# Kernel optimization log

Measured on AMD Instinct MI355X. Metric: run time of the kernel, lower is better.

Reference implementation:

```python
import jax, jax.numpy as jnp
import numpy as np

B, T, H, NH = 4, 2048, 1024, 16
HD = H // NH  # 64


def setup_inputs() -> dict:
    key = jax.random.key(0)
    ks = jax.random.split(key, 8)
    s = 0.02
    return {
        "hidden_states": jax.random.normal(ks[0], (B, T, H), dtype=jnp.float32),
        "attention_mask": jnp.zeros((B, 1, 1, T), dtype=jnp.float32),
        "Wq": jax.random.normal(ks[1], (H, H), dtype=jnp.float32) * s,
        "bq": jnp.zeros((H,), dtype=jnp.float32),
        "Wk": jax.random.normal(ks[2], (H, H), dtype=jnp.float32) * s,
        "bk": jnp.zeros((H,), dtype=jnp.float32),
        "Wv": jax.random.normal(ks[3], (H, H), dtype=jnp.float32) * s,
        "bv": jnp.zeros((H,), dtype=jnp.float32),
    }


def _split_heads(x):
    # [B, T, H] -> [B, NH, T, HD]
    b, t, _ = x.shape
    return x.reshape(b, t, NH, HD).transpose(0, 2, 1, 3)


def reference(hidden_states, attention_mask, Wq, bq, Wk, bk, Wv, bv):
    # QKV projections (torch Linear: x @ W.T + b)
    q = _split_heads(hidden_states @ Wq.T + bq)
    k = _split_heads(hidden_states @ Wk.T + bk)
    v = _split_heads(hidden_states @ Wv.T + bv)

    scale = HD ** (-0.5)
    # [B, NH, T, T]
    scores = jnp.einsum("bhqd,bhkd->bhqk", q, k) * scale
    t = q.shape[2]
    causal = jnp.triu(jnp.ones((t, t), dtype=bool), k=1)
    scores = jnp.where(causal[None, None], -jnp.inf, scores)
    scores = scores + attention_mask  # additive mask [B,1,1,T]
    probs = jax.nn.softmax(scores, axis=-1)
    # dropout is identity in eval mode
    out = jnp.einsum("bhqk,bhkd->bhqd", probs, v)
    # [B, NH, T, HD] -> [B, T, H]
    return out.transpose(0, 2, 1, 3).reshape(hidden_states.shape[0], t, H)
```

## Files before the change

kernel.cpp:

```cpp
#include <hip/hip_runtime.h>
#include <math.h>

#define B_  4
#define T_  2048
#define H_  1024
#define NH_ 16
#define HD_ 64

typedef __bf16  bf16x8  __attribute__((ext_vector_type(8)));
typedef float   f32x4   __attribute__((ext_vector_type(4)));
typedef unsigned short ushort8v __attribute__((ext_vector_type(8)));
typedef short   short4v __attribute__((ext_vector_type(4)));

__device__ __forceinline__ unsigned short f2bf(float f) {
    unsigned int u = __builtin_bit_cast(unsigned int, f);
    u += 0x7fffu + ((u >> 16) & 1u);
    return (unsigned short)(u >> 16);
}

__device__ __forceinline__ f32x4 mfma16x16x16bf16(short4v a, short4v b, f32x4 c) {
#if __has_builtin(__builtin_amdgcn_mfma_f32_16x16x16bf16_1k)
    return __builtin_amdgcn_mfma_f32_16x16x16bf16_1k(a, b, c, 0, 0, 0);
#else
    f32x4 d = c;
    asm volatile("v_mfma_f32_16x16x16_bf16 %0, %1, %2, %0\n\ts_nop 7\n\ts_nop 7"
                 : "+v"(d) : "v"(a), "v"(b));
    return d;
#endif
}

__device__ __forceinline__ void gload_lds16(const unsigned short* g,
                                            unsigned short* l) {
    __builtin_amdgcn_global_load_lds(
        (const __attribute__((address_space(1))) unsigned int*)g,
        (__attribute__((address_space(3))) unsigned int*)l, 16, 0, 0);
}

#define SBARRIER()   asm volatile("s_barrier" ::: "memory")
#define LGKMCNT0()   asm volatile("s_waitcnt lgkmcnt(0)" ::: "memory")
#define VMCNT6()     asm volatile("s_waitcnt vmcnt(6)" ::: "memory")
#define VMCNT0()     asm volatile("s_waitcnt vmcnt(0)" ::: "memory")

__global__ void cvt_f32_bf16(const float* __restrict__ in,
                             unsigned short* __restrict__ out, int n8) {
    int stride = gridDim.x * blockDim.x;
    for (int i = blockIdx.x * blockDim.x + threadIdx.x; i < n8; i += stride) {
        const float4* p = reinterpret_cast<const float4*>(in) + (size_t)i * 2;
        float4 f0 = p[0], f1 = p[1];
        ushort8v o;
        o[0] = f2bf(f0.x); o[1] = f2bf(f0.y); o[2] = f2bf(f0.z); o[3] = f2bf(f0.w);
        o[4] = f2bf(f1.x); o[5] = f2bf(f1.y); o[6] = f2bf(f1.z); o[7] = f2bf(f1.w);
        reinterpret_cast<ushort8v*>(out)[i] = o;
    }
}

__global__ void cvt_w3(const float* __restrict__ Wq, const float* __restrict__ Wk,
                       const float* __restrict__ Wv,
                       unsigned short* __restrict__ oq, unsigned short* __restrict__ ok,
                       unsigned short* __restrict__ ov, int n8) {
    const int z = blockIdx.y;
    const float* in = (z == 0) ? Wq : (z == 1) ? Wk : Wv;
    unsigned short* out = (z == 0) ? oq : (z == 1) ? ok : ov;
    int stride = gridDim.x * blockDim.x;
    for (int i = blockIdx.x * blockDim.x + threadIdx.x; i < n8; i += stride) {
        const float4* p = reinterpret_cast<const float4*>(in) + (size_t)i * 2;
        float4 f0 = p[0], f1 = p[1];
        ushort8v o;
        o[0] = f2bf(f0.x); o[1] = f2bf(f0.y); o[2] = f2bf(f0.z); o[3] = f2bf(f0.w);
        o[4] = f2bf(f1.x); o[5] = f2bf(f1.y); o[6] = f2bf(f1.z); o[7] = f2bf(f1.w);
        reinterpret_cast<ushort8v*>(out)[i] = o;
    }
}

__global__ __launch_bounds__(512) void qkv_gemm_all(
    const unsigned short* __restrict__ X,
    const unsigned short* __restrict__ Wq,
    const unsigned short* __restrict__ Wk,
    const unsigned short* __restrict__ Wv,
    const float* __restrict__ bq,
    const float* __restrict__ bk,
    const float* __restrict__ bv,
    unsigned short* __restrict__ Qo,
    unsigned short* __restrict__ Ko,
    unsigned short* __restrict__ Vo)
{
    const int id     = blockIdx.x;
    const int xcd    = id & 7;
    const int within = id >> 3;
    const int z      = within >> 5;
    const int rest   = within & 31;
    const int xb     = rest & 7;
    const int yb     = xcd * 4 + (rest >> 3);

    const unsigned short* W = (z == 0) ? Wq : (z == 1) ? Wk : Wv;
    const float* bias = (z == 0) ? bq : (z == 1) ? bk : bv;
    unsigned short* out = (z == 0) ? Qo : (z == 1) ? Ko : Vo;

    const int K = 1024;
    const int t    = threadIdx.x;
    const int lane = t & 63;
    const int wid  = t >> 6;
    const int lo = lane & 15, hi = lane >> 4;
    const int wm = wid >> 1, wn = wid & 1;
    const int m0 = yb * 256;
    const int n0 = xb * 128;

    __shared__ unsigned short As[2][256 * 64];
    __shared__ unsigned short Bs[2][128 * 64];

    const int srowoff = lane >> 3;
    const int scol    = lane & 7;

    f32x4 acc[4][4];
#pragma unroll
    for (int i = 0; i < 4; ++i)
#pragma unroll
        for (int j = 0; j < 4; ++j) acc[i][j] = (f32x4){0.f, 0.f, 0.f, 0.f};

#define STAGE_(AS, BS, KOFF)                                                  \
    do {                                                                      \
        _Pragma("unroll") for (int p = 0; p < 4; ++p) {                       \
            const int rowb = p * 64 + wid * 8;                                \
            const int row  = rowb + srowoff;                                  \
            const int c16  = scol ^ (row & 7);                                \
            gload_lds16(&X[(size_t)(m0 + row) * K + (KOFF) + c16 * 8],        \
                        &(AS)[rowb * 64]);                                    \
        }                                                                     \
        _Pragma("unroll") for (int p = 0; p < 2; ++p) {                       \
            const int rowb = p * 64 + wid * 8;                                \
            const int row  = rowb + srowoff;                                  \
            const int c16  = scol ^ (row & 7);                                \
            gload_lds16(&W[(size_t)(n0 + row) * K + (KOFF) + c16 * 8],        \
                        &(BS)[rowb * 64]);                                    \
        }                                                                     \
    } while (0)

#define KTILE_(AS, BS, HAVE_NEXT, KOFF_NEXT)                                  \
    do {                                                                      \
        bf16x8 a[4][2], bfr[4][2];                                            \
        _Pragma("unroll") for (int mt = 0; mt < 4; ++mt)                      \
            _Pragma("unroll") for (int ks = 0; ks < 2; ++ks)                  \
                a[mt][ks] = *reinterpret_cast<const bf16x8*>(                 \
                    &(AS)[(wm * 64 + mt * 16 + lo) * 64 +                     \
                          (((ks * 4 + hi) ^ (lo & 7)) * 8)]);                 \
        _Pragma("unroll") for (int nt = 0; nt < 4; ++nt)                      \
            _Pragma("unroll") for (int ks = 0; ks < 2; ++ks)                  \
                bfr[nt][ks] = *reinterpret_cast<const bf16x8*>(               \
                    &(BS)[(wn * 64 + nt * 16 + lo) * 64 +                     \
                          (((ks * 4 + hi) ^ (lo & 7)) * 8)]);                 \
        LGKMCNT0();                                                           \
        SBARRIER();                     \
        if (HAVE_NEXT) STAGE_(AS, BS, KOFF_NEXT);      \
        __builtin_amdgcn_s_setprio(1);                                        \
        _Pragma("unroll") for (int mt = 0; mt < 4; ++mt)                      \
            _Pragma("unroll") for (int nt = 0; nt < 4; ++nt)                  \
                acc[mt][nt] = __builtin_amdgcn_mfma_f32_16x16x32_bf16(        \
                    a[mt][0], bfr[nt][0], acc[mt][nt], 0, 0, 0);              \
        _Pragma("unroll") for (int mt = 0; mt < 4; ++mt)                      \
            _Pragma("unroll") for (int nt = 0; nt < 4; ++nt)                  \
                acc[mt][nt] = __builtin_amdgcn_mfma_f32_16x16x32_bf16(        \
                    a[mt][1], bfr[nt][1], acc[mt][nt], 0, 0, 0);              \
        __builtin_amdgcn_s_setprio(0);                                        \
        if (HAVE_NEXT) VMCNT6(); else VMCNT0();                               \
        SBARRIER();                          \
    } while (0)

    STAGE_(As[0], Bs[0], 0);
    STAGE_(As[1], Bs[1], 64);
    VMCNT6();
    SBARRIER();

#pragma unroll
    for (int k0 = 0; k0 < K; k0 += 128) {
        KTILE_(As[0], Bs[0], (k0 + 128 < K), k0 + 128);
        KTILE_(As[1], Bs[1], (k0 + 192 < K), k0 + 192);
    }

#pragma unroll
    for (int nt = 0; nt < 4; ++nt) {
        int n = n0 + wn * 64 + nt * 16 + lo;
        float bv_ = bias[n];
        int h = n >> 6, d = n & 63;
#pragma unroll
        for (int mt = 0; mt < 4; ++mt) {
            int mbase = m0 + wm * 64 + mt * 16 + hi * 4;
            int bb = mbase >> 11;
            int tt = mbase & 2047;
            int ct = (tt >> 4) & 3;
            size_t tilebase = ((size_t)(bb * NH_ + h) * 32 + (tt >> 6)) * 4096;
            if (z == 2) {
                ushort4 pk;
                pk.x = f2bf(acc[mt][nt][0] + bv_);
                pk.y = f2bf(acc[mt][nt][1] + bv_);
                pk.z = f2bf(acc[mt][nt][2] + bv_);
                pk.w = f2bf(acc[mt][nt][3] + bv_);
                *reinterpret_cast<ushort4*>(
                    &out[tilebase + (size_t)ct * 1024 + (size_t)(hi * 16 + lo) * 16 + nt * 4]) = pk;
            } else if (z == 1) {
                const int ksd = d >> 5;
                const int hif = (d >> 3) & 3;
                const int jd  = d & 7;
                size_t fragbase = tilebase + (size_t)(ct * 2 + ksd) * 512;
#pragma unroll
                for (int r = 0; r < 4; ++r)
                    out[fragbase + (size_t)(hif * 16 + hi * 4 + r) * 8 + jd] =
                        f2bf(acc[mt][nt][r] + bv_);
            } else {
                size_t base = (size_t)(bb * NH_ + h) * T_;
#pragma unroll
                for (int r = 0; r < 4; ++r)
                    out[(base + tt + r) * HD_ + d] = f2bf(acc[mt][nt][r] + bv_);
            }
        }
    }
#undef STAGE_
#undef KTILE_
}

__global__ __launch_bounds__(128, 2) void attn_fwd15(
    const unsigned short* __restrict__ Q,
    const unsigned short* __restrict__ Kf,
    const unsigned short* __restrict__ Vf,
    const float* __restrict__ amask,
    float* __restrict__ out)
{
    const float SC    = 0.125f * 1.44269504089f;
    const float LOG2E = 1.44269504089f;

    const int lane = threadIdx.x & 63;
    const int w    = threadIdx.x >> 6;
    const int lo = lane & 15, hi = lane >> 4;

    const int bid    = blockIdx.x;
    const int xcd    = bid & 7;
    const int within = bid >> 3;
    const int bh     = xcd * 8 + (within & 7);
    const int u      = 63 - (within >> 3);
    const int b      = bh >> 4;
    const int h      = bh & 15;

    const unsigned short* Qg = Q + (size_t)bh * T_ * HD_;
    const float* am = amask + (size_t)b * T_;
    float* outBase = out + (size_t)b * T_ * H_ + h * HD_;

    __shared__ f32x4 Lo[2][4][64];
    __shared__ float Ll[2][64];

    const int q0   = u * 32;
    const int nt   = (u >> 1) + 1;
    const int half = nt >> 1;
    const int ktBeg = w ? half : 0;
    const int ktEnd = w ? nt : half;

    bf16x8 qf[2][2];
#pragma unroll
    for (int mt = 0; mt < 2; ++mt)
#pragma unroll
        for (int ks = 0; ks < 2; ++ks)
            qf[mt][ks] = *reinterpret_cast<const bf16x8*>(
                &Qg[(size_t)(q0 + mt * 16 + lo) * HD_ + ks * 32 + hi * 8]);

    f32x4 o[2][4];
#pragma unroll
    for (int mt = 0; mt < 2; ++mt)
#pragma unroll
        for (int dt = 0; dt < 4; ++dt) o[mt][dt] = (f32x4){0.f, 0.f, 0.f, 0.f};
    float l_r[2] = {0.f, 0.f};

    const unsigned short* kp = Kf + ((size_t)bh * 32 + ktBeg) * 4096;
    const unsigned short* vp = Vf + ((size_t)bh * 32 + ktBeg) * 4096;
    const float*          ap = am + ktBeg * 64;

    for (int kt = ktBeg; kt < ktEnd; ++kt, kp += 4096, vp += 4096, ap += 64) {
        const int kv0 = kt * 64;

        bf16x8 kf[4][2];
#pragma unroll
        for (int ct = 0; ct < 4; ++ct)
#pragma unroll
            for (int ks = 0; ks < 2; ++ks)
                kf[ct][ks] = *reinterpret_cast<const bf16x8*>(
                    &kp[(ct * 2 + ks) * 512 + lane * 8]);

        short4v vf[4][4];
#pragma unroll
        for (int ct = 0; ct < 4; ++ct) {
            union { ushort8v u8; short4v s4[2]; } va, vb;
            va.u8 = *reinterpret_cast<const ushort8v*>(&vp[ct * 1024 + lane * 16]);
            vb.u8 = *reinterpret_cast<const ushort8v*>(&vp[ct * 1024 + lane * 16 + 8]);
            vf[0][ct] = va.s4[0];
            vf[1][ct] = va.s4[1];
            vf[2][ct] = vb.s4[0];
            vf[3][ct] = vb.s4[1];
        }

        f32x4 amv[4];
#pragma unroll
        for (int ct = 0; ct < 4; ++ct)
            amv[ct] = *reinterpret_cast<const f32x4*>(&ap[ct * 16 + hi * 4]) * LOG2E;

        f32x4 s[2][4];
#pragma unroll
        for (int mt = 0; mt < 2; ++mt)
#pragma unroll
            for (int ct = 0; ct < 4; ++ct) s[mt][ct] = (f32x4){0.f, 0.f, 0.f, 0.f};
#pragma unroll
        for (int ks = 0; ks < 2; ++ks)
#pragma unroll
            for (int ct = 0; ct < 4; ++ct)
#pragma unroll
                for (int mt = 0; mt < 2; ++mt)
                    s[mt][ct] = __builtin_amdgcn_mfma_f32_16x16x32_bf16(
                        kf[ct][ks], qf[mt][ks], s[mt][ct], 0, 0, 0);

        const bool edge = (kv0 + 63 > q0);

        short4v p[2][4];
#pragma unroll
        for (int mt = 0; mt < 2; ++mt) {
            f32x4 rsv = (f32x4){0.f, 0.f, 0.f, 0.f};
#pragma unroll
            for (int ct = 0; ct < 4; ++ct) {
                f32x4 sv;
#pragma unroll
                for (int r = 0; r < 4; ++r)
                    sv[r] = fmaf(s[mt][ct][r], SC, amv[ct][r]);
                if (edge) {
                    const int q = q0 + mt * 16 + lo;
#pragma unroll
                    for (int r = 0; r < 4; ++r)
                        if (kv0 + ct * 16 + hi * 4 + r > q) sv[r] = -INFINITY;
                }
                short4v pk;
#pragma unroll
                for (int r = 0; r < 4; ++r) {
                    float pe = exp2f(sv[r]);
                    rsv[r] += pe;
                    __bf16 hb = (__bf16)pe;
                    pk[r] = __builtin_bit_cast(short, hb);
                }
                p[mt][ct] = pk;
            }
            l_r[mt] += (rsv[0] + rsv[1]) + (rsv[2] + rsv[3]);
        }

#pragma unroll
        for (int ct = 0; ct < 4; ++ct)
#pragma unroll
            for (int mt = 0; mt < 2; ++mt)
#pragma unroll
                for (int dt = 0; dt < 4; ++dt)
                    o[mt][dt] = mfma16x16x16bf16(vf[dt][ct], p[mt][ct], o[mt][dt]);
    }

    if (w == 1) {
#pragma unroll
        for (int mt = 0; mt < 2; ++mt) {
            Ll[mt][lane] = l_r[mt];
#pragma unroll
            for (int dt = 0; dt < 4; ++dt)
                Lo[mt][dt][lane] = o[mt][dt];
        }
    }
    __syncthreads();
    if (w == 0) {
#pragma unroll
        for (int mt = 0; mt < 2; ++mt) {
            float lf = l_r[mt] + Ll[mt][lane];
            lf += __shfl_xor(lf, 16, 64);
            lf += __shfl_xor(lf, 32, 64);
            const float inv = 1.0f / lf;
            const int tq = q0 + mt * 16 + lo;
            float* orow = outBase + (size_t)tq * H_;
#pragma unroll
            for (int dt = 0; dt < 4; ++dt) {
                f32x4 v = (o[mt][dt] + Lo[mt][dt][lane]) * inv;
                *reinterpret_cast<f32x4*>(&orow[dt * 16 + hi * 4]) = v;
            }
        }
    }
}

extern "C" void kernel_launch(void* const* d_in, const int* in_sizes, int n_in,
                              void* d_out, int out_size, void* d_ws, size_t ws_size,
                              hipStream_t stream) {
    const float* hs    = (const float*)d_in[0];
    const float* amask = (const float*)d_in[1];
    const float* Wq    = (const float*)d_in[2];
    const float* bq    = (const float*)d_in[3];
    const float* Wk    = (const float*)d_in[4];
    const float* bk    = (const float*)d_in[5];
    const float* Wv    = (const float*)d_in[6];
    const float* bv    = (const float*)d_in[7];
    float* out = (float*)d_out;

    unsigned short* Xbf = (unsigned short*)d_ws;
    unsigned short* Wqb = Xbf + (size_t)8192 * 1024;
    unsigned short* Wkb = Wqb + (size_t)1024 * 1024;
    unsigned short* Wvb = Wkb + (size_t)1024 * 1024;
    unsigned short* Qb  = Wvb + (size_t)1024 * 1024;
    unsigned short* Kfb = Qb  + (size_t)B_ * NH_ * T_ * HD_;
    unsigned short* Vfb = Kfb + (size_t)B_ * NH_ * T_ * HD_;

    cvt_f32_bf16<<<4096, 256, 0, stream>>>(hs, Xbf, (8192 * 1024) / 8);
    dim3 gw(512, 3);
    cvt_w3<<<gw, 256, 0, stream>>>(Wq, Wk, Wv, Wqb, Wkb, Wvb, (1024 * 1024) / 8);

    qkv_gemm_all<<<768, 512, 0, stream>>>(Xbf, Wqb, Wkb, Wvb, bq, bk, bv,
                                          Qb, Kfb, Vfb);

    attn_fwd15<<<4096, 128, 0, stream>>>(Qb, Kfb, Vfb, amask, out);
}
```

Baseline: 153.8 us.

## Rebalance causal attention with paired query tiles per wave and prefetched K

The attention kernel now gives each wave two query tiles, u and 63-u, so every wave does roughly the same causal work. This replaces splitting the KV range between two waves and merging the partial results through shared memory and a barrier. K fragments and mask values are double-buffered so the next tile's loads are issued before the current tile's compute. The grid shrinks to 1024 blocks with launch bounds of one block per SIMD, and the two fp32-to-bf16 conversion launches are merged into one. This trades parallelism and occupancy for better load balance and less synchronization.

```diff
diff --git a/kernel.cpp b/kernel.cpp
--- a/kernel.cpp
+++ b/kernel.cpp
@@ -41,35 +41,33 @@
 #define VMCNT6()     asm volatile("s_waitcnt vmcnt(6)" ::: "memory")
 #define VMCNT0()     asm volatile("s_waitcnt vmcnt(0)" ::: "memory")
 
-__global__ void cvt_f32_bf16(const float* __restrict__ in,
-                             unsigned short* __restrict__ out, int n8) {
-    int stride = gridDim.x * blockDim.x;
-    for (int i = blockIdx.x * blockDim.x + threadIdx.x; i < n8; i += stride) {
-        const float4* p = reinterpret_cast<const float4*>(in) + (size_t)i * 2;
-        float4 f0 = p[0], f1 = p[1];
-        ushort8v o;
-        o[0] = f2bf(f0.x); o[1] = f2bf(f0.y); o[2] = f2bf(f0.z); o[3] = f2bf(f0.w);
-        o[4] = f2bf(f1.x); o[5] = f2bf(f1.y); o[6] = f2bf(f1.z); o[7] = f2bf(f1.w);
-        reinterpret_cast<ushort8v*>(out)[i] = o;
+__global__ void cvt_all(const float* __restrict__ hs,
+                        const float* __restrict__ Wq,
+                        const float* __restrict__ Wk,
+                        const float* __restrict__ Wv,
+                        unsigned short* __restrict__ Xo,
+                        unsigned short* __restrict__ oq,
+                        unsigned short* __restrict__ ok,
+                        unsigned short* __restrict__ ov) {
+    const int bid = blockIdx.x;
+    const float* in;
+    unsigned short* out;
+    int i;
+    if (bid < 4096) {
+        in = hs; out = Xo; i = bid * 256 + threadIdx.x;
+    } else {
+        const int r = bid - 4096;
+        const int z = r >> 9;
+        in  = (z == 0) ? Wq : (z == 1) ? Wk : Wv;
+        out = (z == 0) ? oq : (z == 1) ? ok : ov;
+        i = (r & 511) * 256 + threadIdx.x;
     }
-}
-
-__global__ void cvt_w3(const float* __restrict__ Wq, const float* __restrict__ Wk,
-                       const float* __restrict__ Wv,
-                       unsigned short* __restrict__ oq, unsigned short* __restrict__ ok,
-                       unsigned short* __restrict__ ov, int n8) {
-    const int z = blockIdx.y;
-    const float* in = (z == 0) ? Wq : (z == 1) ? Wk : Wv;
-    unsigned short* out = (z == 0) ? oq : (z == 1) ? ok : ov;
-    int stride = gridDim.x * blockDim.x;
-    for (int i = blockIdx.x * blockDim.x + threadIdx.x; i < n8; i += stride) {
-        const float4* p = reinterpret_cast<const float4*>(in) + (size_t)i * 2;
-        float4 f0 = p[0], f1 = p[1];
-        ushort8v o;
-        o[0] = f2bf(f0.x); o[1] = f2bf(f0.y); o[2] = f2bf(f0.z); o[3] = f2bf(f0.w);
-        o[4] = f2bf(f1.x); o[5] = f2bf(f1.y); o[6] = f2bf(f1.z); o[7] = f2bf(f1.w);
-        reinterpret_cast<ushort8v*>(out)[i] = o;
-    }
+    const float4* p = reinterpret_cast<const float4*>(in) + (size_t)i * 2;
+    float4 f0 = p[0], f1 = p[1];
+    ushort8v o;
+    o[0] = f2bf(f0.x); o[1] = f2bf(f0.y); o[2] = f2bf(f0.z); o[3] = f2bf(f0.w);
+    o[4] = f2bf(f1.x); o[5] = f2bf(f1.y); o[6] = f2bf(f1.z); o[7] = f2bf(f1.w);
+    reinterpret_cast<ushort8v*>(out)[i] = o;
 }
 
 __global__ __launch_bounds__(512) void qkv_gemm_all(
@@ -149,8 +147,8 @@
                     &(BS)[(wn * 64 + nt * 16 + lo) * 64 +                     \
                           (((ks * 4 + hi) ^ (lo & 7)) * 8)]);                 \
         LGKMCNT0();                                                           \
-        SBARRIER();                     \
-        if (HAVE_NEXT) STAGE_(AS, BS, KOFF_NEXT);      \
+        SBARRIER();                                                           \
+        if (HAVE_NEXT) STAGE_(AS, BS, KOFF_NEXT);                             \
         __builtin_amdgcn_s_setprio(1);                                        \
         _Pragma("unroll") for (int mt = 0; mt < 4; ++mt)                      \
             _Pragma("unroll") for (int nt = 0; nt < 4; ++nt)                  \
@@ -162,7 +160,7 @@
                     a[mt][1], bfr[nt][1], acc[mt][nt], 0, 0, 0);              \
         __builtin_amdgcn_s_setprio(0);                                        \
         if (HAVE_NEXT) VMCNT6(); else VMCNT0();                               \
-        SBARRIER();                          \
+        SBARRIER();                                                           \
     } while (0)
 
     STAGE_(As[0], Bs[0], 0);
@@ -217,7 +215,75 @@
 #undef KTILE_
 }
 
-__global__ __launch_bounds__(128, 2) void attn_fwd15(
+
+#define AKLOAD_(KF, AMV)                                                      \
+    do {                                                                      \
+        _Pragma("unroll") for (int ct = 0; ct < 4; ++ct)                      \
+            _Pragma("unroll") for (int ks = 0; ks < 2; ++ks)                  \
+                KF[ct][ks] = *reinterpret_cast<const bf16x8*>(                \
+                    &kp[(ct * 2 + ks) * 512 + lane * 8]);                     \
+        _Pragma("unroll") for (int ct = 0; ct < 4; ++ct)                      \
+            AMV[ct] = *reinterpret_cast<const f32x4*>(                        \
+                          &ap[ct * 16 + hi * 4]) * LOG2E;                     \
+        kp += 4096; ap += 64;                                                 \
+    } while (0)
+
+#define ABODY_(KF, AMV, KV0)                                                  \
+    do {                                                                      \
+        const int kv0_ = (KV0);                                               \
+        short4v vf[4][4];                                                     \
+        _Pragma("unroll") for (int ct = 0; ct < 4; ++ct) {                    \
+            union { ushort8v u8; short4v s4[2]; } va, vb;                     \
+            va.u8 = *reinterpret_cast<const ushort8v*>(                       \
+                &vp[ct * 1024 + lane * 16]);                                  \
+            vb.u8 = *reinterpret_cast<const ushort8v*>(                       \
+                &vp[ct * 1024 + lane * 16 + 8]);                              \
+            vf[0][ct] = va.s4[0]; vf[1][ct] = va.s4[1];                       \
+            vf[2][ct] = vb.s4[0]; vf[3][ct] = vb.s4[1];                       \
+        }                                                                     \
+        f32x4 s[2][4];                                                        \
+        _Pragma("unroll") for (int mt = 0; mt < 2; ++mt)                      \
+            _Pragma("unroll") for (int ct = 0; ct < 4; ++ct)                  \
+                s[mt][ct] = (f32x4){0.f, 0.f, 0.f, 0.f};                      \
+        _Pragma("unroll") for (int ks = 0; ks < 2; ++ks)                      \
+            _Pragma("unroll") for (int ct = 0; ct < 4; ++ct)                  \
+                _Pragma("unroll") for (int mt = 0; mt < 2; ++mt)              \
+                    s[mt][ct] = __builtin_amdgcn_mfma_f32_16x16x32_bf16(      \
+                        KF[ct][ks], qf[mt][ks], s[mt][ct], 0, 0, 0);          \
+        const bool edge = (kv0_ + 63 > q0);                                   \
+        short4v p[2][4];                                                      \
+        _Pragma("unroll") for (int mt = 0; mt < 2; ++mt) {                    \
+            f32x4 rsv = (f32x4){0.f, 0.f, 0.f, 0.f};                          \
+            _Pragma("unroll") for (int ct = 0; ct < 4; ++ct) {                \
+                f32x4 sv;                                                     \
+                _Pragma("unroll") for (int r = 0; r < 4; ++r)                 \
+                    sv[r] = fmaf(s[mt][ct][r], SC, AMV[ct][r]);               \
+                if (edge) {                                                   \
+                    const int q = q0 + mt * 16 + lo;                          \
+                    _Pragma("unroll") for (int r = 0; r < 4; ++r)             \
+                        if (kv0_ + ct * 16 + hi * 4 + r > q)                  \
+                            sv[r] = -INFINITY;                                \
+                }                                                             \
+                short4v pk;                                                   \
+                _Pragma("unroll") for (int r = 0; r < 4; ++r) {               \
+                    float pe = exp2f(sv[r]);                                  \
+                    rsv[r] += pe;                                             \
+                    __bf16 hb = (__bf16)pe;                                   \
+                    pk[r] = __builtin_bit_cast(short, hb);                    \
+                }                                                             \
+                p[mt][ct] = pk;                                               \
+            }                                                                 \
+            l_r[mt] += (rsv[0] + rsv[1]) + (rsv[2] + rsv[3]);                 \
+        }                                                                     \
+        _Pragma("unroll") for (int ct = 0; ct < 4; ++ct)                      \
+            _Pragma("unroll") for (int mt = 0; mt < 2; ++mt)                  \
+                _Pragma("unroll") for (int dt = 0; dt < 4; ++dt)              \
+                    o[mt][dt] = mfma16x16x16bf16(vf[dt][ct], p[mt][ct],       \
+                                                 o[mt][dt]);                  \
+        vp += 4096;                                                           \
+    } while (0)
+
+__global__ __launch_bounds__(128, 1) void attn_fwd16(
     const unsigned short* __restrict__ Q,
     const unsigned short* __restrict__ Kf,
     const unsigned short* __restrict__ Vf,
@@ -235,7 +301,7 @@
     const int xcd    = bid & 7;
     const int within = bid >> 3;
     const int bh     = xcd * 8 + (within & 7);
-    const int u      = 63 - (within >> 3);
+    const int up     = ((within >> 3) << 1) + w;
     const int b      = bh >> 4;
     const int h      = bh & 15;
 
@@ -243,130 +309,50 @@
     const float* am = amask + (size_t)b * T_;
     float* outBase = out + (size_t)b * T_ * H_ + h * HD_;
 
-    __shared__ f32x4 Lo[2][4][64];
-    __shared__ float Ll[2][64];
-
-    const int q0   = u * 32;
-    const int nt   = (u >> 1) + 1;
-    const int half = nt >> 1;
-    const int ktBeg = w ? half : 0;
-    const int ktEnd = w ? nt : half;
-
-    bf16x8 qf[2][2];
-#pragma unroll
-    for (int mt = 0; mt < 2; ++mt)
-#pragma unroll
-        for (int ks = 0; ks < 2; ++ks)
-            qf[mt][ks] = *reinterpret_cast<const bf16x8*>(
-                &Qg[(size_t)(q0 + mt * 16 + lo) * HD_ + ks * 32 + hi * 8]);
-
-    f32x4 o[2][4];
-#pragma unroll
-    for (int mt = 0; mt < 2; ++mt)
-#pragma unroll
-        for (int dt = 0; dt < 4; ++dt) o[mt][dt] = (f32x4){0.f, 0.f, 0.f, 0.f};
-    float l_r[2] = {0.f, 0.f};
-
-    const unsigned short* kp = Kf + ((size_t)bh * 32 + ktBeg) * 4096;
-    const unsigned short* vp = Vf + ((size_t)bh * 32 + ktBeg) * 4096;
-    const float*          ap = am + ktBeg * 64;
-
-    for (int kt = ktBeg; kt < ktEnd; ++kt, kp += 4096, vp += 4096, ap += 64) {
-        const int kv0 = kt * 64;
-
-        bf16x8 kf[4][2];
-#pragma unroll
-        for (int ct = 0; ct < 4; ++ct)
+#pragma unroll
+    for (int seg = 0; seg < 2; ++seg) {
+        const int u  = seg ? (63 - up) : up;
+        const int q0 = u * 32;
+        const int ntT = (u >> 1) + 1;
+
+        bf16x8 qf[2][2];
+#pragma unroll
+        for (int mt = 0; mt < 2; ++mt)
 #pragma unroll
             for (int ks = 0; ks < 2; ++ks)
-                kf[ct][ks] = *reinterpret_cast<const bf16x8*>(
-                    &kp[(ct * 2 + ks) * 512 + lane * 8]);
-
-        short4v vf[4][4];
-#pragma unroll
-        for (int ct = 0; ct < 4; ++ct) {
-            union { ushort8v u8; short4v s4[2]; } va, vb;
-            va.u8 = *reinterpret_cast<const ushort8v*>(&vp[ct * 1024 + lane * 16]);
-            vb.u8 = *reinterpret_cast<const ushort8v*>(&vp[ct * 1024 + lane * 16 + 8]);
-            vf[0][ct] = va.s4[0];
-            vf[1][ct] = va.s4[1];
-            vf[2][ct] = vb.s4[0];
-            vf[3][ct] = vb.s4[1];
+                qf[mt][ks] = *reinterpret_cast<const bf16x8*>(
+                    &Qg[(size_t)(q0 + mt * 16 + lo) * HD_ + ks * 32 + hi * 8]);
+
+        f32x4 o[2][4];
+#pragma unroll
+        for (int mt = 0; mt < 2; ++mt)
+#pragma unroll
+            for (int dt = 0; dt < 4; ++dt) o[mt][dt] = (f32x4){0.f, 0.f, 0.f, 0.f};
+        float l_r[2] = {0.f, 0.f};
+
+        const unsigned short* kp = Kf + (size_t)bh * 32 * 4096;
+        const unsigned short* vp = Vf + (size_t)bh * 32 * 4096;
+        const float*          ap = am;
+
+        bf16x8 kfA[4][2], kfB[4][2];
+        f32x4  amvA[4], amvB[4];
+
+        AKLOAD_(kfA, amvA);
+        int kt = 0, kv0 = 0;
+        for (;;) {
+            if (kt + 1 < ntT) AKLOAD_(kfB, amvB);
+            ABODY_(kfA, amvA, kv0);
+            if (++kt == ntT) break;
+            kv0 += 64;
+            if (kt + 1 < ntT) AKLOAD_(kfA, amvA);
+            ABODY_(kfB, amvB, kv0);
+            if (++kt == ntT) break;
+            kv0 += 64;
         }
 
-        f32x4 amv[4];
-#pragma unroll
-        for (int ct = 0; ct < 4; ++ct)
-            amv[ct] = *reinterpret_cast<const f32x4*>(&ap[ct * 16 + hi * 4]) * LOG2E;
-
-        f32x4 s[2][4];
-#pragma unroll
-        for (int mt = 0; mt < 2; ++mt)
-#pragma unroll
-            for (int ct = 0; ct < 4; ++ct) s[mt][ct] = (f32x4){0.f, 0.f, 0.f, 0.f};
-#pragma unroll
-        for (int ks = 0; ks < 2; ++ks)
-#pragma unroll
-            for (int ct = 0; ct < 4; ++ct)
-#pragma unroll
-                for (int mt = 0; mt < 2; ++mt)
-                    s[mt][ct] = __builtin_amdgcn_mfma_f32_16x16x32_bf16(
-                        kf[ct][ks], qf[mt][ks], s[mt][ct], 0, 0, 0);
-
-        const bool edge = (kv0 + 63 > q0);
-
-        short4v p[2][4];
 #pragma unroll
         for (int mt = 0; mt < 2; ++mt) {
-            f32x4 rsv = (f32x4){0.f, 0.f, 0.f, 0.f};
-#pragma unroll
-            for (int ct = 0; ct < 4; ++ct) {
-                f32x4 sv;
-#pragma unroll
-                for (int r = 0; r < 4; ++r)
-                    sv[r] = fmaf(s[mt][ct][r], SC, amv[ct][r]);
-                if (edge) {
-                    const int q = q0 + mt * 16 + lo;
-#pragma unroll
-                    for (int r = 0; r < 4; ++r)
-                        if (kv0 + ct * 16 + hi * 4 + r > q) sv[r] = -INFINITY;
-                }
-                short4v pk;
-#pragma unroll
-                for (int r = 0; r < 4; ++r) {
-                    float pe = exp2f(sv[r]);
-                    rsv[r] += pe;
-                    __bf16 hb = (__bf16)pe;
-                    pk[r] = __builtin_bit_cast(short, hb);
-                }
-                p[mt][ct] = pk;
-            }
-            l_r[mt] += (rsv[0] + rsv[1]) + (rsv[2] + rsv[3]);
-        }
-
-#pragma unroll
-        for (int ct = 0; ct < 4; ++ct)
-#pragma unroll
-            for (int mt = 0; mt < 2; ++mt)
-#pragma unroll
-                for (int dt = 0; dt < 4; ++dt)
-                    o[mt][dt] = mfma16x16x16bf16(vf[dt][ct], p[mt][ct], o[mt][dt]);
-    }
-
-    if (w == 1) {
-#pragma unroll
-        for (int mt = 0; mt < 2; ++mt) {
-            Ll[mt][lane] = l_r[mt];
-#pragma unroll
-            for (int dt = 0; dt < 4; ++dt)
-                Lo[mt][dt][lane] = o[mt][dt];
-        }
-    }
-    __syncthreads();
-    if (w == 0) {
-#pragma unroll
-        for (int mt = 0; mt < 2; ++mt) {
-            float lf = l_r[mt] + Ll[mt][lane];
+            float lf = l_r[mt];
             lf += __shfl_xor(lf, 16, 64);
             lf += __shfl_xor(lf, 32, 64);
             const float inv = 1.0f / lf;
@@ -374,7 +360,7 @@
             float* orow = outBase + (size_t)tq * H_;
 #pragma unroll
             for (int dt = 0; dt < 4; ++dt) {
-                f32x4 v = (o[mt][dt] + Lo[mt][dt][lane]) * inv;
+                f32x4 v = o[mt][dt] * inv;
                 *reinterpret_cast<f32x4*>(&orow[dt * 16 + hi * 4]) = v;
             }
         }
@@ -402,12 +388,10 @@
     unsigned short* Kfb = Qb  + (size_t)B_ * NH_ * T_ * HD_;
     unsigned short* Vfb = Kfb + (size_t)B_ * NH_ * T_ * HD_;
 
-    cvt_f32_bf16<<<4096, 256, 0, stream>>>(hs, Xbf, (8192 * 1024) / 8);
-    dim3 gw(512, 3);
-    cvt_w3<<<gw, 256, 0, stream>>>(Wq, Wk, Wv, Wqb, Wkb, Wvb, (1024 * 1024) / 8);
+    cvt_all<<<5632, 256, 0, stream>>>(hs, Wq, Wk, Wv, Xbf, Wqb, Wkb, Wvb);
 
     qkv_gemm_all<<<768, 512, 0, stream>>>(Xbf, Wqb, Wkb, Wvb, bq, bk, bv,
                                           Qb, Kfb, Vfb);
 
-    attn_fwd15<<<4096, 128, 0, stream>>>(Qb, Kfb, Vfb, amask, out);
-}
+    attn_fwd16<<<1024, 128, 0, stream>>>(Qb, Kfb, Vfb, amask, out);
+}
```

Result: slower. 179.5 us (+16.7%).
